# Kernel tuning notes

Measured on AMD Instinct MI355X. Metric: run time of the kernel, lower is better.

The kernel has to match this reference:

```python
import jax, jax.numpy as jnp
import numpy as np
from jax import lax

N_LAYER = 4
D_MODEL = 1024
D_INNER = 2048   # expand=2
D_STATE = 16
DT_RANK = 64     # ceil(d_model/16)
D_CONV = 4
BATCH = 2
SEQ = 2048
EPS = 1e-5


def setup_inputs() -> dict:
    key = jax.random.key(0)
    ks = jax.random.split(key, 8)
    rn = lambda k, shape, s=0.02: jax.random.normal(k, shape, dtype=jnp.float32) * s
    # S4D-real init for A_log, as in mamba_ssm
    A_init = jnp.tile(jnp.arange(1, D_STATE + 1, dtype=jnp.float32)[None, None, :],
                      (N_LAYER, D_INNER, 1))
    return {
        "hidden_states": jax.random.normal(ks[0], (BATCH, SEQ, D_MODEL), dtype=jnp.float32),
        "norm_w": jnp.ones((N_LAYER, D_MODEL), jnp.float32),
        "norm_b": jnp.zeros((N_LAYER, D_MODEL), jnp.float32),
        "in_proj_w": rn(ks[1], (N_LAYER, 2 * D_INNER, D_MODEL)),
        "conv_w": rn(ks[2], (N_LAYER, D_INNER, D_CONV), 0.1),
        "conv_b": jnp.zeros((N_LAYER, D_INNER), jnp.float32),
        "x_proj_w": rn(ks[3], (N_LAYER, DT_RANK + 2 * D_STATE, D_INNER)),
        "dt_proj_w": rn(ks[4], (N_LAYER, D_INNER, DT_RANK), 0.1),
        "dt_proj_b": rn(ks[5], (N_LAYER, D_INNER), 0.1),
        "A_log": jnp.log(A_init),
        "D": jnp.ones((N_LAYER, D_INNER), jnp.float32),
        "out_proj_w": rn(ks[6], (N_LAYER, D_MODEL, D_INNER)),
        "final_norm_w": jnp.ones((D_MODEL,), jnp.float32),
        "final_norm_b": jnp.zeros((D_MODEL,), jnp.float32),
    }


def _layernorm(x, w, b):
    mu = jnp.mean(x, axis=-1, keepdims=True)
    var = jnp.mean(jnp.square(x - mu), axis=-1, keepdims=True)
    return (x - mu) * lax.rsqrt(var + EPS) * w + b


def _mamba_block(h, in_w, conv_w, conv_b, x_w, dt_w, dt_b, A_log, Dp, out_w):
    B, L, _ = h.shape
    xz = jnp.einsum('bld,ed->ble', h, in_w)               # [B,L,2*d_inner]
    x, z = jnp.split(xz, 2, axis=-1)
    # depthwise causal conv1d (kernel D_CONV), truncated to L
    xp = jnp.pad(x, ((0, 0), (D_CONV - 1, 0), (0, 0)))
    x = sum(xp[:, k:k + L, :] * conv_w[:, k] for k in range(D_CONV)) + conv_b
    x = jax.nn.silu(x)
    x_dbl = jnp.einsum('bld,ed->ble', x, x_w)             # [B,L,dt_rank+2*d_state]
    dt, Bm, Cm = jnp.split(x_dbl, [DT_RANK, DT_RANK + D_STATE], axis=-1)
    delta = jax.nn.softplus(jnp.einsum('blr,dr->bld', dt, dt_w) + dt_b)  # [B,L,d_inner]
    A = -jnp.exp(A_log)                                   # [d_inner, d_state]

    def step(state, xs):
        d_t, B_t, C_t, u_t = xs                           # [B,di],[B,ds],[B,ds],[B,di]
        dA = jnp.exp(d_t[..., None] * A)                  # [B,di,ds]
        state = dA * state + (d_t * u_t)[..., None] * B_t[:, None, :]
        y_t = jnp.einsum('bds,bs->bd', state, C_t)
        return state, y_t

    xs = (jnp.swapaxes(delta, 0, 1), jnp.swapaxes(Bm, 0, 1),
          jnp.swapaxes(Cm, 0, 1), jnp.swapaxes(x, 0, 1))
    init = jnp.zeros((B, D_INNER, D_STATE), dtype=h.dtype)
    _, ys = lax.scan(step, init, xs)                      # ys: [L,B,di]
    y = jnp.swapaxes(ys, 0, 1) + x * Dp
    y = y * jax.nn.silu(z)
    return jnp.einsum('bld,ed->ble', y, out_w)            # [B,L,d_model]


def reference(hidden_states, norm_w, norm_b, in_proj_w, conv_w, conv_b,
              x_proj_w, dt_proj_w, dt_proj_b, A_log, D, out_proj_w,
              final_norm_w, final_norm_b):
    residual = None
    for i in range(N_LAYER):
        residual = hidden_states + residual if residual is not None else hidden_states
        h = _layernorm(residual, norm_w[i], norm_b[i])
        hidden_states = _mamba_block(h, in_proj_w[i], conv_w[i], conv_b[i],
                                     x_proj_w[i], dt_proj_w[i], dt_proj_b[i],
                                     A_log[i], D[i], out_proj_w[i])
    residual = hidden_states + residual
    return _layernorm(residual, final_norm_w, final_norm_b)
```

## Files before the change

### kernel.cpp

```cpp
#include <hip/hip_runtime.h>
#include <math.h>

#define N_LAYERS 4
#define DMODEL 1024
#define DINNER 2048
#define DSTATE 16
#define DTRANK 64
#define DCONV 4
#define NBATCH 2
#define LSEQ 2048
#define LNEPS 1e-5f
#define ROWS (NBATCH * LSEQ)
#define CLEN 32
#define NCHUNK (LSEQ / CLEN)
#define XP 128
#define KSLICE 512
#define NSLICE (DINNER / KSLICE)

typedef __attribute__((ext_vector_type(8))) short bf16x8;
typedef __attribute__((ext_vector_type(8))) unsigned short ushort8;
typedef __attribute__((ext_vector_type(4))) float f32x4;
typedef __attribute__((ext_vector_type(4))) unsigned int uint4v;

__device__ __forceinline__ unsigned short f2bf(float f) {
  unsigned int u = __float_as_uint(f);
  return (unsigned short)((u + 0x7FFFu + ((u >> 16) & 1u)) >> 16);
}
__device__ __forceinline__ float bf2f(unsigned short h) {
  return __uint_as_float(((unsigned int)h) << 16);
}

__device__ __forceinline__ void gload16(const unsigned short* g, unsigned short* l) {
  __builtin_amdgcn_global_load_lds(
      (const __attribute__((address_space(1))) unsigned int*)g,
      (__attribute__((address_space(3))) unsigned int*)l, 16, 0, 0);
}

__device__ __forceinline__ float softplus_f(float x) {
  float e = __expf(-fabsf(x));
  return fmaxf(x, 0.f) + __logf(1.f + e);
}

__global__ __launch_bounds__(256) void cvt_f2bf(const float* __restrict__ src,
                                                unsigned short* __restrict__ dst, int n4) {
  int i = blockIdx.x * 256 + threadIdx.x;
  if (i >= n4) return;
  float4 v = ((const float4*)src)[i];
  ushort4 o;
  o.x = f2bf(v.x); o.y = f2bf(v.y); o.z = f2bf(v.z); o.w = f2bf(v.w);
  ((ushort4*)dst)[i] = o;
}

__global__ __launch_bounds__(256) void cvt_xpw(const float* __restrict__ src,
                                               unsigned short* __restrict__ dst) {
  int i = blockIdx.x * 256 + threadIdx.x;
  int col4 = i & 511;
  int row = (i >> 9) & 127;
  int layer = i >> 16;
  float4 v = make_float4(0.f, 0.f, 0.f, 0.f);
  if (row < 96) v = ((const float4*)(src + ((size_t)layer * 96 + row) * 2048))[col4];
  ushort4 o;
  o.x = f2bf(v.x); o.y = f2bf(v.y); o.z = f2bf(v.z); o.w = f2bf(v.w);
  ((ushort4*)(dst + ((size_t)layer * 128 + row) * 2048))[col4] = o;
}

template<bool OBF>
__global__ __launch_bounds__(256) void ln_kernel(
    const float* __restrict__ src, float* __restrict__ res_copy,
    const float* __restrict__ w, const float* __restrict__ b, void* out) {
  int row = blockIdx.x;
  int t = threadIdx.x;
  const float4* srow = (const float4*)(src + (size_t)row * DMODEL);
  float4 v = srow[t];
  if (res_copy) ((float4*)(res_copy + (size_t)row * DMODEL))[t] = v;
  float s = v.x + v.y + v.z + v.w;
  float sq = v.x * v.x + v.y * v.y + v.z * v.z + v.w * v.w;
  #pragma unroll
  for (int o = 32; o >= 1; o >>= 1) {
    s += __shfl_xor(s, o);
    sq += __shfl_xor(sq, o);
  }
  __shared__ float ss[4], ssq[4];
  int wid = t >> 6, lane = t & 63;
  if (lane == 0) { ss[wid] = s; ssq[wid] = sq; }
  __syncthreads();
  s = ss[0] + ss[1] + ss[2] + ss[3];
  sq = ssq[0] + ssq[1] + ssq[2] + ssq[3];
  float mu = s * (1.f / DMODEL);
  float var = sq * (1.f / DMODEL) - mu * mu;
  float rs = rsqrtf(var + LNEPS);
  float4 wv = ((const float4*)w)[t];
  float4 bv = ((const float4*)b)[t];
  float4 o4;
  o4.x = (v.x - mu) * rs * wv.x + bv.x;
  o4.y = (v.y - mu) * rs * wv.y + bv.y;
  o4.z = (v.z - mu) * rs * wv.z + bv.z;
  o4.w = (v.w - mu) * rs * wv.w + bv.w;
  if (OBF) {
    ushort4 ob;
    ob.x = f2bf(o4.x); ob.y = f2bf(o4.y); ob.z = f2bf(o4.z); ob.w = f2bf(o4.w);
    ((ushort4*)((unsigned short*)out + (size_t)row * DMODEL))[t] = ob;
  } else {
    ((float4*)((float*)out + (size_t)row * DMODEL))[t] = o4;
  }
}

template<int ACT, bool BIAS, bool ADD, bool WF32, bool WBF>
__global__ __launch_bounds__(512) void gemm256(
    const unsigned short* __restrict__ A, int lda,
    const unsigned short* __restrict__ W, int ldw,
    float* __restrict__ C, int ldc, int K,
    const float* __restrict__ bias,
    const float* __restrict__ addsrc,
    unsigned short* __restrict__ Cb) {
  __shared__ unsigned short lds[2][2][256][64];
  const int t = threadIdx.x;
  const int lane = t & 63;
  const int wave = t >> 6;
  const int wr = wave >> 2;
  const int wc = wave & 3;
  const int m0 = blockIdx.y * 256, n0 = blockIdx.x * 256;

  const int srow = t >> 3;
  const int sslot = t & 7;
  const int frow = lane & 15;
  const int hi = lane >> 4;

  f32x4 acc[8][4];
  #pragma unroll
  for (int m = 0; m < 8; m++)
    #pragma unroll
    for (int n = 0; n < 4; n++) acc[m][n] = (f32x4){0.f, 0.f, 0.f, 0.f};

  const int NT = K / 64;

  auto stage = [&](int buf, int kt) {
    const int scol = (sslot << 3) + kt * 64;
    #pragma unroll
    for (int r = 0; r < 4; ++r) {
      int row = srow + (r << 6);
      gload16(A + (size_t)(m0 + row) * lda + scol, &lds[buf][0][row][sslot << 3]);
    }
    #pragma unroll
    for (int r = 0; r < 4; ++r) {
      int row = srow + (r << 6);
      gload16(W + (size_t)(n0 + row) * ldw + scol, &lds[buf][1][row][sslot << 3]);
    }
  };

  auto compute = [&](int buf) {
    #pragma unroll
    for (int ks = 0; ks < 2; ++ks) {
      bf16x8 a[8], b[4];
      #pragma unroll
      for (int m = 0; m < 8; ++m) {
        int row = wr * 128 + m * 16 + frow;
        a[m] = *(const bf16x8*)&lds[buf][0][row][(ks * 4 + hi) << 3];
      }
      #pragma unroll
      for (int n = 0; n < 4; ++n) {
        int row = wc * 64 + n * 16 + frow;
        b[n] = *(const bf16x8*)&lds[buf][1][row][(ks * 4 + hi) << 3];
      }
      __builtin_amdgcn_s_setprio(1);
      #pragma unroll
      for (int m = 0; m < 8; ++m)
        #pragma unroll
        for (int n = 0; n < 4; ++n)
          acc[m][n] = __builtin_amdgcn_mfma_f32_16x16x32_bf16(a[m], b[n], acc[m][n], 0, 0, 0);
      __builtin_amdgcn_s_setprio(0);
    }
  };

  stage(0, 0);
  if (NT > 1) stage(1, 1);
  for (int kt = 0; kt < NT - 1; ++kt) {
    asm volatile("s_waitcnt vmcnt(8)" ::: "memory");
    __builtin_amdgcn_s_barrier();
    asm volatile("" ::: "memory");
    compute(kt & 1);
    __builtin_amdgcn_s_barrier();
    asm volatile("" ::: "memory");
    if (kt + 2 < NT) stage(kt & 1, kt + 2);
  }
  asm volatile("s_waitcnt vmcnt(0)" ::: "memory");
  __builtin_amdgcn_s_barrier();
  asm volatile("" ::: "memory");
  compute((NT - 1) & 1);

  #pragma unroll
  for (int m = 0; m < 8; ++m) {
    int rbase = m0 + wr * 128 + m * 16 + hi * 4;
    #pragma unroll
    for (int n = 0; n < 4; ++n) {
      int ccol = n0 + wc * 64 + n * 16 + frow;
      #pragma unroll
      for (int j = 0; j < 4; ++j) {
        int crow = rbase + j;
        float v = acc[m][n][j];
        if (BIAS) v += bias[ccol];
        if (ACT == 1) v = softplus_f(v);
        if (ADD) v += addsrc[(size_t)crow * ldc + ccol];
        if (WF32) C[(size_t)crow * ldc + ccol] = v;
        if (WBF) Cb[(size_t)crow * ldc + ccol] = f2bf(v);
      }
    }
  }
}

template<int ACT, bool BIAS, bool ADD, bool WF32, bool WBF, bool PARTIAL>
__global__ __launch_bounds__(256) void gemm_bf16(
    const unsigned short* __restrict__ A, int lda,
    const unsigned short* __restrict__ W, int ldw,
    float* __restrict__ C, int ldc, int K,
    const float* __restrict__ bias,
    const float* __restrict__ addsrc,
    unsigned short* __restrict__ Cb) {
  __shared__ unsigned short As[2][128][32];
  __shared__ unsigned short Ws[2][128][32];
  int t = threadIdx.x;
  int lane = t & 63, wave = t >> 6;
  int wr = wave >> 1, wc = wave & 1;
  int m0 = blockIdx.y * 128, n0 = blockIdx.x * 128;

  int kbase = 0;
  if (PARTIAL) {
    kbase = blockIdx.z * K;
    C += (size_t)blockIdx.z * (size_t)gridDim.y * 128 * ldc;
  }

  int r0 = t >> 2;
  int kk8 = (t & 3) << 3;
  const unsigned short* Ag = A + (size_t)(m0 + r0) * lda + kbase + kk8;
  const unsigned short* Wg = W + (size_t)(n0 + r0) * ldw + kbase + kk8;
  const size_t Astep = (size_t)64 * lda;
  const size_t Wstep = (size_t)64 * ldw;

  f32x4 zero = {0.f, 0.f, 0.f, 0.f};
  f32x4 acc[4][4];
  #pragma unroll
  for (int m = 0; m < 4; m++)
    #pragma unroll
    for (int n = 0; n < 4; n++) acc[m][n] = zero;

  int frow = lane & 15;
  int fk = (lane >> 4) << 3;

  auto stage = [&](int buf, int kt) {
    const unsigned short* ag = Ag + kt * 32;
    const unsigned short* wg = Wg + kt * 32;
    unsigned short* la = &As[buf][r0][kk8];
    unsigned short* lw = &Ws[buf][r0][kk8];
    gload16(ag, la);
    gload16(ag + Astep, la + 64 * 32);
    gload16(wg, lw);
    gload16(wg + Wstep, lw + 64 * 32);
  };
  auto compute = [&](int buf) {
    bf16x8 af[4], bw[4];
    #pragma unroll
    for (int m = 0; m < 4; m++)
      af[m] = *(const bf16x8*)&As[buf][wr * 64 + m * 16 + frow][fk];
    #pragma unroll
    for (int n = 0; n < 4; n++)
      bw[n] = *(const bf16x8*)&Ws[buf][wc * 64 + n * 16 + frow][fk];
    #pragma unroll
    for (int m = 0; m < 4; m++)
      #pragma unroll
      for (int n = 0; n < 4; n++)
        acc[m][n] = __builtin_amdgcn_mfma_f32_16x16x32_bf16(af[m], bw[n], acc[m][n], 0, 0, 0);
  };

  const int NT = K / 32;
  stage(0, 0);
  __syncthreads();
  int cur = 0;
  for (int kt = 0; kt < NT - 1; ++kt) {
    stage(cur ^ 1, kt + 1);
    compute(cur);
    __syncthreads();
    cur ^= 1;
  }
  compute(cur);

  #pragma unroll
  for (int m = 0; m < 4; m++) {
    int rbase = m0 + wr * 64 + m * 16 + ((lane >> 4) << 2);
    #pragma unroll
    for (int n = 0; n < 4; n++) {
      int ccol = n0 + wc * 64 + n * 16 + (lane & 15);
      #pragma unroll
      for (int j = 0; j < 4; j++) {
        int crow = rbase + j;
        float v = acc[m][n][j];
        if (BIAS) v += bias[ccol];
        if (ACT == 1) v = softplus_f(v);
        if (ADD) v += addsrc[(size_t)crow * ldc + ccol];
        if (WF32 || PARTIAL) C[(size_t)crow * ldc + ccol] = v;
        if (WBF) Cb[(size_t)crow * ldc + ccol] = f2bf(v);
      }
    }
  }
}

__global__ __launch_bounds__(256) void combine_xdbl(
    const float* __restrict__ part, float* __restrict__ xdbl,
    unsigned short* __restrict__ xdbl_bf) {
  int i = blockIdx.x * 256 + threadIdx.x;
  const size_t slab = (size_t)ROWS * XP / 4;
  const float4* p = (const float4*)part;
  float4 a = p[i], b = p[i + slab], c = p[i + 2 * slab], d = p[i + 3 * slab];
  float4 s;
  s.x = a.x + b.x + c.x + d.x;
  s.y = a.y + b.y + c.y + d.y;
  s.z = a.z + b.z + c.z + d.z;
  s.w = a.w + b.w + c.w + d.w;
  ((float4*)xdbl)[i] = s;
  ushort4 o;
  o.x = f2bf(s.x); o.y = f2bf(s.y); o.z = f2bf(s.z); o.w = f2bf(s.w);
  ((ushort4*)xdbl_bf)[i] = o;
}

__global__ __launch_bounds__(256) void conv_silu_kernel(
    const unsigned short* __restrict__ xz, const float* __restrict__ cw,
    const float* __restrict__ cb, unsigned short* __restrict__ xbf) {
  int tid = blockIdx.x * 256 + threadIdx.x;
  int dv = tid & (DINNER / 8 - 1);
  int rg = tid >> 8;
  int l0 = (rg & (LSEQ / 4 - 1)) * 4;
  int row0 = rg * 4;
  int d = dv * 8;

  float4 wq[8];
  #pragma unroll
  for (int j = 0; j < 8; j++) wq[j] = ((const float4*)(cw + (size_t)d * DCONV))[j];
  float4 b0 = ((const float4*)(cb + d))[0];
  float4 b1 = ((const float4*)(cb + d))[1];
  const float bias[8] = {b0.x, b0.y, b0.z, b0.w, b1.x, b1.y, b1.z, b1.w};

  ushort8 xin[7];
  #pragma unroll
  for (int r = 0; r < 7; r++) {
    int l = l0 - 3 + r;
    if (l >= 0)
      xin[r] = *(const ushort8*)(xz + (size_t)(row0 - 3 + r) * (2 * DINNER) + d);
    else
      xin[r] = (ushort8){0, 0, 0, 0, 0, 0, 0, 0};
  }

  #pragma unroll
  for (int o = 0; o < 4; o++) {
    ushort8 ob;
    #pragma unroll
    for (int j = 0; j < 8; j++) {
      const float* wj = (const float*)&wq[j];
      float acc = bias[j];
      #pragma unroll
      for (int k = 0; k < DCONV; k++)
        acc = fmaf(bf2f(xin[o + k][j]), wj[k], acc);
      float s = acc / (1.f + __expf(-acc));
      ob[j] = f2bf(s);
    }
    *(ushort8*)(xbf + (size_t)(row0 + o) * DINNER + d) = ob;
  }
}

__global__ __launch_bounds__(256) void scan_p1(
    const float* __restrict__ delta, const unsigned short* __restrict__ u,
    const float* __restrict__ xdbl, const float* __restrict__ A_log,
    unsigned int* __restrict__ carrybuf) {
  int tid = blockIdx.x * 256 + threadIdx.x;
  int t = threadIdx.x;
  int d = tid & (DINNER - 1);
  int chunk = (tid >> 11) & (NCHUNK - 1);
  int b = tid >> 17;
  int l0 = chunk * CLEN;

  __shared__ float bl[CLEN][16];
  {
    const float4* src4 = (const float4*)(xdbl + ((size_t)b * LSEQ + l0) * XP);
    if (t < CLEN * 4) {
      int li = t >> 2, qi = t & 3;
      ((float4*)&bl[li][0])[qi] = src4[li * (XP / 4) + 16 + qi];
    }
  }
  __syncthreads();

  float A[DSTATE], st[DSTATE], ap[DSTATE];
  const float4* Ar = (const float4*)(A_log + d * DSTATE);
  #pragma unroll
  for (int q = 0; q < 4; q++) {
    float4 av = Ar[q];
    A[4 * q] = -__expf(av.x); A[4 * q + 1] = -__expf(av.y);
    A[4 * q + 2] = -__expf(av.z); A[4 * q + 3] = -__expf(av.w);
  }
  #pragma unroll
  for (int s = 0; s < DSTATE; s++) { st[s] = 0.f; ap[s] = 1.f; }

  const float* dptr = delta + ((size_t)b * LSEQ + l0) * DINNER + d;
  const unsigned short* uptr = u + ((size_t)b * LSEQ + l0) * DINNER + d;
  float dt_n = dptr[0];
  float uu_n = bf2f(uptr[0]);
  #pragma unroll 4
  for (int l = 0; l < CLEN; l++) {
    float dt = dt_n, uu = uu_n;
    if (l + 1 < CLEN) {
      dt_n = dptr[(size_t)(l + 1) * DINNER];
      uu_n = bf2f(uptr[(size_t)(l + 1) * DINNER]);
    }
    float du = dt * uu;
    #pragma unroll
    for (int q = 0; q < 4; q++) {
      float4 B4 = *(const float4*)&bl[l][q * 4];
      const float Bj[4] = {B4.x, B4.y, B4.z, B4.w};
      #pragma unroll
      for (int j = 0; j < 4; j++) {
        int s = 4 * q + j;
        float dA = __expf(dt * A[s]);
        st[s] = fmaf(dA, st[s], du * Bj[j]);
        ap[s] *= dA;
      }
    }
  }
  uint4v* co = (uint4v*)(carrybuf + (size_t)tid * DSTATE);
  #pragma unroll
  for (int q = 0; q < 4; q++) {
    uint4v v;
    #pragma unroll
    for (int j = 0; j < 4; j++)
      v[j] = ((unsigned int)f2bf(ap[4 * q + j]) << 16) | f2bf(st[4 * q + j]);
    co[q] = v;
  }
}

__global__ __launch_bounds__(256) void scan_p2(
    const unsigned int* __restrict__ cbuf, unsigned short* __restrict__ carryin) {
  int tid = blockIdx.x * 256 + threadIdx.x;
  int ds = tid & (DINNER * DSTATE - 1);
  int b = tid >> 15;
  float carry = 0.f;
  size_t base = (size_t)b * NCHUNK * DINNER * DSTATE + ds;
  const size_t cs = DINNER * DSTATE;
  for (int c = 0; c < NCHUNK; c += 4) {
    size_t i0 = base + (size_t)c * cs;
    unsigned int v0 = cbuf[i0], v1 = cbuf[i0 + cs];
    unsigned int v2 = cbuf[i0 + 2 * cs], v3 = cbuf[i0 + 3 * cs];
    carryin[i0] = f2bf(carry);
    carry = fmaf(bf2f(v0 >> 16), carry, bf2f(v0 & 0xFFFFu));
    carryin[i0 + cs] = f2bf(carry);
    carry = fmaf(bf2f(v1 >> 16), carry, bf2f(v1 & 0xFFFFu));
    carryin[i0 + 2 * cs] = f2bf(carry);
    carry = fmaf(bf2f(v2 >> 16), carry, bf2f(v2 & 0xFFFFu));
    carryin[i0 + 3 * cs] = f2bf(carry);
    carry = fmaf(bf2f(v3 >> 16), carry, bf2f(v3 & 0xFFFFu));
  }
}

__global__ __launch_bounds__(256) void scan_p3(
    const float* __restrict__ delta, const unsigned short* __restrict__ u,
    const float* __restrict__ xdbl, const unsigned short* __restrict__ xzbf,
    const float* __restrict__ A_log, const float* __restrict__ Dp,
    const unsigned short* __restrict__ carryin, unsigned short* __restrict__ ybf) {
  int tid = blockIdx.x * 256 + threadIdx.x;
  int t = threadIdx.x;
  int d = tid & (DINNER - 1);
  int chunk = (tid >> 11) & (NCHUNK - 1);
  int b = tid >> 17;
  int l0 = chunk * CLEN;

  __shared__ float bc[CLEN][32];
  {
    const float4* src4 = (const float4*)(xdbl + ((size_t)b * LSEQ + l0) * XP);
    int li = t >> 3, qi = t & 7;
    ((float4*)&bc[li][0])[qi] = src4[li * (XP / 4) + 16 + qi];
  }
  __syncthreads();

  float A[DSTATE], st[DSTATE];
  {
    const ushort8* ci8 = (const ushort8*)(carryin + (size_t)tid * DSTATE);
    ushort8 c0 = ci8[0], c1 = ci8[1];
    #pragma unroll
    for (int j = 0; j < 8; j++) { st[j] = bf2f(c0[j]); st[8 + j] = bf2f(c1[j]); }
  }
  const float4* Ar = (const float4*)(A_log + d * DSTATE);
  #pragma unroll
  for (int q = 0; q < 4; q++) {
    float4 av = Ar[q];
    A[4 * q] = -__expf(av.x); A[4 * q + 1] = -__expf(av.y);
    A[4 * q + 2] = -__expf(av.z); A[4 * q + 3] = -__expf(av.w);
  }
  float Dval = Dp[d];

  const float* dptr = delta + ((size_t)b * LSEQ + l0) * DINNER + d;
  const unsigned short* uptr = u + ((size_t)b * LSEQ + l0) * DINNER + d;
  const unsigned short* zptr = xzbf + ((size_t)b * LSEQ + l0) * (2 * DINNER) + DINNER + d;
  unsigned short* yptr = ybf + ((size_t)b * LSEQ + l0) * DINNER + d;

  float dt_n = dptr[0];
  float uu_n = bf2f(uptr[0]);
  float zz_n = bf2f(zptr[0]);
  #pragma unroll 4
  for (int l = 0; l < CLEN; l++) {
    float dt = dt_n, uu = uu_n, zz = zz_n;
    if (l + 1 < CLEN) {
      dt_n = dptr[(size_t)(l + 1) * DINNER];
      uu_n = bf2f(uptr[(size_t)(l + 1) * DINNER]);
      zz_n = bf2f(zptr[(size_t)(l + 1) * (2 * DINNER)]);
    }
    float du = dt * uu;
    #pragma unroll
    for (int q = 0; q < 4; q++) {
      float4 B4 = *(const float4*)&bc[l][q * 4];
      const float Bj[4] = {B4.x, B4.y, B4.z, B4.w};
      #pragma unroll
      for (int j = 0; j < 4; j++) {
        int s = 4 * q + j;
        float dA = __expf(dt * A[s]);
        st[s] = fmaf(dA, st[s], du * Bj[j]);
      }
    }
    float acc = 0.f;
    #pragma unroll
    for (int q = 0; q < 4; q++) {
      float4 C4 = *(const float4*)&bc[l][16 + q * 4];
      const float Cj[4] = {C4.x, C4.y, C4.z, C4.w};
      #pragma unroll
      for (int j = 0; j < 4; j++) acc = fmaf(st[4 * q + j], Cj[j], acc);
    }
    float yv = (acc + uu * Dval) * (zz / (1.f + __expf(-zz)));
    yptr[(size_t)l * DINNER] = f2bf(yv);
  }
}

extern "C" void kernel_launch(void* const* d_in, const int* in_sizes, int n_in,
                              void* d_out, int out_size, void* d_ws, size_t ws_size,
                              hipStream_t stream) {
  const float* hidden    = (const float*)d_in[0];
  const float* norm_w    = (const float*)d_in[1];
  const float* norm_b    = (const float*)d_in[2];
  const float* in_proj_w = (const float*)d_in[3];
  const float* conv_w    = (const float*)d_in[4];
  const float* conv_b    = (const float*)d_in[5];
  const float* x_proj_w  = (const float*)d_in[6];
  const float* dt_proj_w = (const float*)d_in[7];
  const float* dt_proj_b = (const float*)d_in[8];
  const float* A_log     = (const float*)d_in[9];
  const float* Dp        = (const float*)d_in[10];
  const float* out_proj_w= (const float*)d_in[11];
  const float* fnw       = (const float*)d_in[12];
  const float* fnb       = (const float*)d_in[13];
  float* out = (float*)d_out;

  const size_t CARRYSZ = (size_t)NBATCH * NCHUNK * DINNER * DSTATE;

  float* residual = (float*)d_ws;
  float* delta    = residual + (size_t)ROWS * DMODEL;
  float* xdbl     = delta + (size_t)ROWS * DINNER;
  float* fend     = xdbl + (size_t)ROWS * XP;

  unsigned short* xz_bf   = (unsigned short*)fend;
  unsigned short* xbuf_bf = xz_bf + (size_t)ROWS * 2 * DINNER;
  unsigned short* h_bf    = xbuf_bf + (size_t)ROWS * DINNER;
  unsigned short* ybuf_bf = h_bf + (size_t)ROWS * DMODEL;
  unsigned short* xdbl_bf = ybuf_bf + (size_t)ROWS * DINNER;
  unsigned short* xpw_bf  = xdbl_bf + (size_t)ROWS * XP;
  unsigned short* dtw_bf  = xpw_bf + (size_t)N_LAYERS * XP * DINNER;
  unsigned short* ipw_bf  = dtw_bf + (size_t)N_LAYERS * DINNER * DTRANK;
  unsigned short* opw_bf  = ipw_bf + (size_t)2 * DINNER * DMODEL;
  unsigned short* usend   = opw_bf + (size_t)DMODEL * DINNER;

  unsigned int*   carrybuf = (unsigned int*)usend;
  unsigned short* carryin  = (unsigned short*)(carrybuf + CARRYSZ);
  float*          xpart    = delta;

  cvt_xpw<<<N_LAYERS * XP * DINNER / 4 / 256, 256, 0, stream>>>(x_proj_w, xpw_bf);
  {
    int n4 = N_LAYERS * DINNER * DTRANK / 4;
    cvt_f2bf<<<n4 / 256, 256, 0, stream>>>(dt_proj_w, dtw_bf, n4);
  }

  for (int i = 0; i < N_LAYERS; i++) {
    {
      int n4 = 2 * DINNER * DMODEL / 4;
      cvt_f2bf<<<n4 / 256, 256, 0, stream>>>(
          in_proj_w + (size_t)i * 2 * DINNER * DMODEL, ipw_bf, n4);
      n4 = DMODEL * DINNER / 4;
      cvt_f2bf<<<n4 / 256, 256, 0, stream>>>(
          out_proj_w + (size_t)i * DMODEL * DINNER, opw_bf, n4);
    }
    ln_kernel<true><<<ROWS, 256, 0, stream>>>(
        i == 0 ? hidden : residual, i == 0 ? residual : nullptr,
        norm_w + (size_t)i * DMODEL, norm_b + (size_t)i * DMODEL, h_bf);
    {
      dim3 g(2 * DINNER / 256, ROWS / 256);
      gemm256<0, false, false, false, true><<<g, 512, 0, stream>>>(
          h_bf, DMODEL, ipw_bf, DMODEL, nullptr, 2 * DINNER, DMODEL,
          nullptr, nullptr, xz_bf);
    }
    conv_silu_kernel<<<ROWS / 4 * DINNER / 8 / 256, 256, 0, stream>>>(
        xz_bf, conv_w + (size_t)i * DINNER * DCONV, conv_b + (size_t)i * DINNER,
        xbuf_bf);
    {
      dim3 g(1, ROWS / 128, NSLICE);
      gemm_bf16<0, false, false, true, false, true><<<g, 256, 0, stream>>>(
          xbuf_bf, DINNER, xpw_bf + (size_t)i * XP * DINNER, DINNER,
          xpart, XP, KSLICE, nullptr, nullptr, nullptr);
      combine_xdbl<<<ROWS * XP / 4 / 256, 256, 0, stream>>>(xpart, xdbl, xdbl_bf);
    }
    {
      dim3 g(DINNER / 128, ROWS / 128);
      gemm_bf16<1, true, false, true, false, false><<<g, 256, 0, stream>>>(
          xdbl_bf, XP, dtw_bf + (size_t)i * DINNER * DTRANK, DTRANK,
          delta, DINNER, DTRANK, dt_proj_b + (size_t)i * DINNER,
          nullptr, nullptr);
    }
    scan_p1<<<NBATCH * NCHUNK * DINNER / 256, 256, 0, stream>>>(
        delta, xbuf_bf, xdbl, A_log + (size_t)i * DINNER * DSTATE, carrybuf);
    scan_p2<<<NBATCH * DINNER * DSTATE / 256, 256, 0, stream>>>(carrybuf, carryin);
    scan_p3<<<NBATCH * NCHUNK * DINNER / 256, 256, 0, stream>>>(
        delta, xbuf_bf, xdbl, xz_bf, A_log + (size_t)i * DINNER * DSTATE,
        Dp + (size_t)i * DINNER, carryin, ybuf_bf);
    {
      dim3 g(DMODEL / 128, ROWS / 128);
      gemm_bf16<0, false, true, true, false, false><<<g, 256, 0, stream>>>(
          ybuf_bf, DINNER, opw_bf, DINNER,
          residual, DMODEL, DINNER, nullptr, residual, nullptr);
    }
  }
  ln_kernel<false><<<ROWS, 256, 0, stream>>>(residual, nullptr, fnw, fnb, out);
}
```

Before: 918.4 us.

## Deepen gemm_bf16 prefetch pipeline, add MFMA priority and XCD-aware block swizzle

The 128x128 bf16 GEMM now issues two k-tiles of loads up front and waits with explicit vmcnt counts and raw barriers, so loads for tile kt+2 overlap compute on tile kt instead of syncing fully each iteration. MFMA sections are wrapped in s_setprio to favour the compute waves. An optional block-index swizzle, used only for the out_proj GEMM, spreads neighbouring tiles across the eight XCDs to improve L2 locality. The hand-written waitcnt depends on gload16 issuing exactly the expected number of memory ops per stage, so a mismatch could cause races.

```diff
diff --git a/kernel.cpp b/kernel.cpp
--- a/kernel.cpp
+++ b/kernel.cpp
@@ -208,7 +208,7 @@
   }
 }
 
-template<int ACT, bool BIAS, bool ADD, bool WF32, bool WBF, bool PARTIAL>
+template<int ACT, bool BIAS, bool ADD, bool WF32, bool WBF, bool PARTIAL, bool SWZ>
 __global__ __launch_bounds__(256) void gemm_bf16(
     const unsigned short* __restrict__ A, int lda,
     const unsigned short* __restrict__ W, int ldw,
@@ -221,7 +221,16 @@
   int t = threadIdx.x;
   int lane = t & 63, wave = t >> 6;
   int wr = wave >> 1, wc = wave & 1;
-  int m0 = blockIdx.y * 128, n0 = blockIdx.x * 128;
+
+  int bx = blockIdx.x, by = blockIdx.y;
+  if (SWZ) {
+    int nwg = gridDim.x * gridDim.y;
+    int bid = by * gridDim.x + bx;
+    int virt = (bid & 7) * (nwg >> 3) + (bid >> 3);
+    bx = virt % gridDim.x;
+    by = virt / gridDim.x;
+  }
+  int m0 = by * 128, n0 = bx * 128;
 
   int kbase = 0;
   if (PARTIAL) {
@@ -264,24 +273,31 @@
     #pragma unroll
     for (int n = 0; n < 4; n++)
       bw[n] = *(const bf16x8*)&Ws[buf][wc * 64 + n * 16 + frow][fk];
+    __builtin_amdgcn_s_setprio(1);
     #pragma unroll
     for (int m = 0; m < 4; m++)
       #pragma unroll
       for (int n = 0; n < 4; n++)
         acc[m][n] = __builtin_amdgcn_mfma_f32_16x16x32_bf16(af[m], bw[n], acc[m][n], 0, 0, 0);
+    __builtin_amdgcn_s_setprio(0);
   };
 
   const int NT = K / 32;
   stage(0, 0);
-  __syncthreads();
-  int cur = 0;
+  if (NT > 1) stage(1, 1);
   for (int kt = 0; kt < NT - 1; ++kt) {
-    stage(cur ^ 1, kt + 1);
-    compute(cur);
-    __syncthreads();
-    cur ^= 1;
-  }
-  compute(cur);
+    asm volatile("s_waitcnt vmcnt(4)" ::: "memory");
+    __builtin_amdgcn_s_barrier();
+    asm volatile("" ::: "memory");
+    compute(kt & 1);
+    __builtin_amdgcn_s_barrier();
+    asm volatile("" ::: "memory");
+    if (kt + 2 < NT) stage(kt & 1, kt + 2);
+  }
+  asm volatile("s_waitcnt vmcnt(0)" ::: "memory");
+  __builtin_amdgcn_s_barrier();
+  asm volatile("" ::: "memory");
+  compute((NT - 1) & 1);
 
   #pragma unroll
   for (int m = 0; m < 4; m++) {
@@ -603,14 +619,14 @@
         xbuf_bf);
     {
       dim3 g(1, ROWS / 128, NSLICE);
-      gemm_bf16<0, false, false, true, false, true><<<g, 256, 0, stream>>>(
+      gemm_bf16<0, false, false, true, false, true, false><<<g, 256, 0, stream>>>(
           xbuf_bf, DINNER, xpw_bf + (size_t)i * XP * DINNER, DINNER,
           xpart, XP, KSLICE, nullptr, nullptr, nullptr);
       combine_xdbl<<<ROWS * XP / 4 / 256, 256, 0, stream>>>(xpart, xdbl, xdbl_bf);
     }
     {
       dim3 g(DINNER / 128, ROWS / 128);
-      gemm_bf16<1, true, false, true, false, false><<<g, 256, 0, stream>>>(
+      gemm_bf16<1, true, false, true, false, false, false><<<g, 256, 0, stream>>>(
           xdbl_bf, XP, dtw_bf + (size_t)i * DINNER * DTRANK, DTRANK,
           delta, DINNER, DTRANK, dt_proj_b + (size_t)i * DINNER,
           nullptr, nullptr);
@@ -623,7 +639,7 @@
         Dp + (size_t)i * DINNER, carryin, ybuf_bf);
     {
       dim3 g(DMODEL / 128, ROWS / 128);
-      gemm_bf16<0, false, true, true, false, false><<<g, 256, 0, stream>>>(
+      gemm_bf16<0, false, true, true, false, false, true><<<g, 256, 0, stream>>>(
           ybuf_bf, DINNER, opw_bf, DINNER,
           residual, DMODEL, DINNER, nullptr, residual, nullptr);
     }
```

Result: slower. 972.6 us (+5.9%).
